# Kernel optimization log

Hardware: AMD Instinct MI355X
Metric: run time of the kernel (lower is better)

## Reference

```python
import jax, jax.numpy as jnp
import numpy as np
import math

NV, NC, NE = 25000, 12500, 250000
DV_LP = DC_LP = 16
D_IN = 128   # in_var_dim = in_con_dim = in_edge_dim
D_OUT = 128  # out_var_dim = out_con_dim = out_edge_dim
E_WO = 5
EDGE_IN = D_IN + 3 + E_WO       # 136 = num_edge_lp_f_with_ss(8) + in_edge_dim(128)
VAR_COMB = DV_LP + D_IN          # 144
CON_COMB = DC_LP + D_IN          # 144

def _lin(key, din, dout, bias=True):
    k1, k2 = jax.random.split(key)
    W = jax.random.normal(k1, (din, dout), jnp.float32) * 0.05
    if bias:
        return W, jax.random.normal(k2, (dout,), jnp.float32) * 0.05
    return W, None

def setup_inputs():
    key = jax.random.key(0)
    ks = iter(jax.random.split(key, 64))
    d = {}
    d["var_learned_f"] = jax.random.normal(next(ks), (NV, D_IN), jnp.float32)
    d["var_lp_f"] = jax.random.normal(next(ks), (NV, DV_LP), jnp.float32)
    d["con_learned_f"] = jax.random.normal(next(ks), (NC, D_IN), jnp.float32)
    d["con_lp_f"] = jax.random.normal(next(ks), (NC, DC_LP), jnp.float32)
    d["edge_learned_f"] = jax.random.normal(next(ks), (NE, D_IN), jnp.float32)
    d["lo_costs"] = jax.random.normal(next(ks), (NE,), jnp.float32)
    d["hi_costs"] = jax.random.normal(next(ks), (NE,), jnp.float32)
    d["def_mm"] = jax.random.normal(next(ks), (NE,), jnp.float32)
    d["edge_lp_f_wo_ss"] = jax.random.normal(next(ks), (NE, E_WO), jnp.float32)
    # con_updater TransformerConv: src=var_comb(144), dst=con_comb(144), edge(136) -> 128
    d["cu_Wq"], d["cu_bq"] = _lin(next(ks), CON_COMB, D_OUT)
    d["cu_Wk"], d["cu_bk"] = _lin(next(ks), VAR_COMB, D_OUT)
    d["cu_Wv"], d["cu_bv"] = _lin(next(ks), VAR_COMB, D_OUT)
    d["cu_We"], _ = _lin(next(ks), EDGE_IN, D_OUT, bias=False)
    d["cu_Ws"], d["cu_bs"] = _lin(next(ks), CON_COMB, D_OUT)
    # var_updater TransformerConv: src=new con_comb(144), dst=var_comb(144)
    d["vu_Wq"], d["vu_bq"] = _lin(next(ks), VAR_COMB, D_OUT)
    d["vu_Wk"], d["vu_bk"] = _lin(next(ks), CON_COMB, D_OUT)
    d["vu_Wv"], d["vu_bv"] = _lin(next(ks), CON_COMB, D_OUT)
    d["vu_We"], _ = _lin(next(ks), EDGE_IN, D_OUT, bias=False)
    d["vu_Ws"], d["vu_bs"] = _lin(next(ks), VAR_COMB, D_OUT)
    # EdgeUpdater MLPs (hidden = out_edge_dim = 128, num_hidden_layers_edge = 0)
    d["eu_vW1"], d["eu_vb1"] = _lin(next(ks), VAR_COMB, D_OUT)
    d["eu_vW2"], d["eu_vb2"] = _lin(next(ks), D_OUT, D_OUT)
    d["eu_cW1"], d["eu_cb1"] = _lin(next(ks), CON_COMB, D_OUT)
    d["eu_cW2"], d["eu_cb2"] = _lin(next(ks), D_OUT, D_OUT)
    d["eu_eW1"], d["eu_eb1"] = _lin(next(ks), EDGE_IN + 2 * D_OUT, D_OUT)
    d["eu_eW2"], d["eu_eb2"] = _lin(next(ks), D_OUT, D_OUT)
    d["edge_index_var"] = jax.random.randint(next(ks), (NE,), 0, NV)
    d["edge_index_con"] = jax.random.randint(next(ks), (NE,), 0, NC)
    return d

def transformer_conv(x_src, x_dst, src_idx, dst_idx, e,
                     Wq, bq, Wk, bk, Wv, bv, We, Ws, bs, n_dst):
    # PyG TransformerConv, heads=1, edge_dim, aggr='mean', root_weight=True
    C = Wq.shape[1]
    q = x_dst @ Wq + bq                      # [N_dst, C]
    k = x_src @ Wk + bk                      # [N_src, C]
    v = x_src @ Wv + bv
    ee = e @ We                              # [E, C] (lin_edge, no bias)
    kj = k[src_idx] + ee
    alpha = jnp.sum(q[dst_idx] * kj, axis=-1) * (1.0 / math.sqrt(C))  # [E]
    # segment softmax over destination nodes
    amax = jax.ops.segment_max(alpha, dst_idx, num_segments=n_dst)
    ex = jnp.exp(alpha - amax[dst_idx])
    denom = jax.ops.segment_sum(ex, dst_idx, num_segments=n_dst)
    a = ex / denom[dst_idx]
    msg = (v[src_idx] + ee) * a[:, None]
    agg = jax.ops.segment_sum(msg, dst_idx, num_segments=n_dst)
    cnt = jax.ops.segment_sum(jnp.ones_like(alpha), dst_idx, num_segments=n_dst)
    out = agg / jnp.maximum(cnt, 1.0)[:, None]   # aggr='mean'
    return out + x_dst @ Ws + bs                 # skip connection (lin_skip)

def _forward(var_learned_f, var_lp_f, con_learned_f, con_lp_f, edge_learned_f,
             lo_costs, hi_costs, def_mm, edge_lp_f_wo_ss,
             cu_Wq, cu_bq, cu_Wk, cu_bk, cu_Wv, cu_bv, cu_We, cu_Ws, cu_bs,
             vu_Wq, vu_bq, vu_Wk, vu_bk, vu_Wv, vu_bv, vu_We, vu_Ws, vu_bs,
             eu_vW1, eu_vb1, eu_vW2, eu_vb2, eu_cW1, eu_cb1, eu_cW2, eu_cb2,
             eu_eW1, eu_eb1, eu_eW2, eu_eb2,
             edge_index_var, edge_index_con):
    relu = jax.nn.relu
    var_comb = jnp.concatenate([var_learned_f, var_lp_f], axis=1)     # [NV,144]
    con_comb = jnp.concatenate([con_learned_f, con_lp_f], axis=1)     # [NC,144]
    edge_comb = jnp.concatenate([edge_learned_f, lo_costs[:, None], hi_costs[:, None],
                                 def_mm[:, None], edge_lp_f_wo_ss], axis=1)  # [NE,136]
    # con update: messages from vars (edge_index[0]) to cons (edge_index[1])
    con_new = relu(transformer_conv(var_comb, con_comb, edge_index_var, edge_index_con,
                                    edge_comb, cu_Wq, cu_bq, cu_Wk, cu_bk, cu_Wv, cu_bv,
                                    cu_We, cu_Ws, cu_bs, NC))
    con_comb = jnp.concatenate([con_new, con_lp_f], axis=1)
    # var update: flow target_to_source -> messages from cons (edge_index[1]) to vars (edge_index[0])
    var_new = relu(transformer_conv(con_comb, var_comb, edge_index_con, edge_index_var,
                                    edge_comb, vu_Wq, vu_bq, vu_Wk, vu_bk, vu_Wv, vu_bv,
                                    vu_We, vu_Ws, vu_bs, NV))
    var_comb = jnp.concatenate([var_new, var_lp_f], axis=1)
    # edge update: compress nodes, gather to edges, concat, MLP
    vc = relu(relu(var_comb @ eu_vW1 + eu_vb1) @ eu_vW2 + eu_vb2)     # [NV,128]
    cc = relu(relu(con_comb @ eu_cW1 + eu_cb1) @ eu_cW2 + eu_cb2)     # [NC,128]
    h = jnp.concatenate([edge_comb, vc[edge_index_var], cc[edge_index_con]], axis=1)  # [NE,392]
    edge_new = relu(relu(h @ eu_eW1 + eu_eb1) @ eu_eW2 + eu_eb2)
    return var_new, con_new, edge_new

def reference(var_learned_f, var_lp_f, con_learned_f, con_lp_f, edge_learned_f,
              lo_costs, hi_costs, def_mm, edge_lp_f_wo_ss,
              cu_Wq, cu_bq, cu_Wk, cu_bk, cu_Wv, cu_bv, cu_We, cu_Ws, cu_bs,
              vu_Wq, vu_bq, vu_Wk, vu_bk, vu_Wv, vu_bv, vu_We, vu_Ws, vu_bs,
              eu_vW1, eu_vb1, eu_vW2, eu_vb2, eu_cW1, eu_cb1, eu_cW2, eu_cb2,
              eu_eW1, eu_eb1, eu_eW2, eu_eb2,
              edge_index_var, edge_index_con):
    return _forward(var_learned_f, var_lp_f, con_learned_f, con_lp_f, edge_learned_f,
                    lo_costs, hi_costs, def_mm, edge_lp_f_wo_ss,
                    cu_Wq, cu_bq, cu_Wk, cu_bk, cu_Wv, cu_bv, cu_We, cu_Ws, cu_bs,
                    vu_Wq, vu_bq, vu_Wk, vu_bk, vu_Wv, vu_bv, vu_We, vu_Ws, vu_bs,
                    eu_vW1, eu_vb1, eu_vW2, eu_vb2, eu_cW1, eu_cb1, eu_cW2, eu_cb2,
                    eu_eW1, eu_eb1, eu_eW2, eu_eb2,
                    edge_index_var, edge_index_con)
```

## Files before the change

### kernel.cpp

```cpp
#include <hip/hip_runtime.h>
#include <math.h>

#define NVV 25000
#define NCC 12500
#define NEE 250000
#define KP 160

typedef short bf16x8 __attribute__((ext_vector_type(8)));
typedef float f32x4 __attribute__((ext_vector_type(4)));

__device__ __forceinline__ unsigned short f2bf(float f) {
  unsigned u = __float_as_uint(f);
  u += 0x7fffu + ((u >> 16) & 1u);
  return (unsigned short)(u >> 16);
}
__device__ __forceinline__ float bf2f(unsigned short u) {
  return __uint_as_float((unsigned)u << 16);
}
__device__ __forceinline__ void gll16(const unsigned short* g, unsigned short* l) {
  __builtin_amdgcn_global_load_lds(
      (const __attribute__((address_space(1))) unsigned int*)(const void*)g,
      (__attribute__((address_space(3))) unsigned int*)(void*)l, 16, 0, 0);
}

__device__ __forceinline__ void stage_rows64(const unsigned short* __restrict__ X,
                                             unsigned short* As, int row0, int N,
                                             int wave, int lane) {
  #pragma unroll
  for (int j = 0; j < 5; ++j) {
    int inst = wave * 5 + j;
    int L = inst * 1024 + lane * 16;
    int kk = L >> 12;
    int r = (L >> 6) & 63;
    int ks = (L & 63) >> 1;
    int grow = row0 + r; if (grow >= N) grow = N - 1;
    gll16(X + (size_t)grow * KP + kk * 32 + ks, As + inst * 512);
  }
}

template <int MI, int NI>
__device__ __forceinline__ void zero_acc(f32x4 (&acc)[MI][NI]) {
  #pragma unroll
  for (int mi = 0; mi < MI; ++mi)
    #pragma unroll
    for (int ni = 0; ni < NI; ++ni) {
      acc[mi][ni][0] = 0.f; acc[mi][ni][1] = 0.f;
      acc[mi][ni][2] = 0.f; acc[mi][ni][3] = 0.f;
    }
}

template <int MI, int NI>
__device__ __forceinline__ void chunk_mfma_g(const unsigned short* As,
                                             const unsigned short* __restrict__ WT,
                                             f32x4 (&acc)[MI][NI], int kk,
                                             int wm, int wn, int fr, int fq) {
  bf16x8 av[MI], bv[NI];
  #pragma unroll
  for (int mi = 0; mi < MI; ++mi)
    av[mi] = *(const bf16x8*)&As[kk * 2048 + (wm + mi * 16 + fr) * 32 + fq * 8];
  #pragma unroll
  for (int ni = 0; ni < NI; ++ni)
    bv[ni] = *(const bf16x8*)&WT[(size_t)(wn + ni * 16 + fr) * KP + kk * 32 + fq * 8];
  #pragma unroll
  for (int mi = 0; mi < MI; ++mi)
    #pragma unroll
    for (int ni = 0; ni < NI; ++ni)
      acc[mi][ni] = __builtin_amdgcn_mfma_f32_16x16x32_bf16(av[mi], bv[ni],
                                                            acc[mi][ni], 0, 0, 0);
}

struct GJob {
  const unsigned short* X; const unsigned short* WT;
  const float* bias; const float* addf;
  float* outf; unsigned short* outb;
  int outb_stride, pad_flag, N, relu_flag;
  int ntf;
};
struct GBatch { GJob j[4]; int start[4]; int njobs; };

__global__ __launch_bounds__(256, 4) void gemm_batch(GBatch B) {
  int job = 0;
  #pragma unroll
  for (int t = 1; t < 4; ++t)
    if (t < B.njobs && (int)blockIdx.x >= B.start[t]) job = t;
  GJob g = B.j[job];
  __shared__ unsigned short As[5 * 64 * 32];
  const int tid = threadIdx.x;
  const int lane = tid & 63, wave = tid >> 6;
  const int row0 = (blockIdx.x - B.start[job]) * 64;
  const int wm = (wave & 1) * 32, wn = (wave >> 1) * 64;
  const int fr = lane & 15, fq = lane >> 4;

  stage_rows64(g.X, As, row0, g.N, wave, lane);
  f32x4 acc[2][4];
  zero_acc<2, 4>(acc);
  __syncthreads();
  #pragma unroll
  for (int kk = 0; kk < 5; ++kk) chunk_mfma_g<2, 4>(As, g.WT, acc, kk, wm, wn, fr, fq);

  #pragma unroll
  for (int mi = 0; mi < 2; ++mi) {
    #pragma unroll
    for (int ni = 0; ni < 4; ++ni) {
      int gcol = wn + ni * 16 + fr;
      float bvv = g.bias ? g.bias[gcol] : 0.0f;
      #pragma unroll
      for (int r = 0; r < 4; ++r) {
        int grow = row0 + wm + mi * 16 + fq * 4 + r;
        if (grow < g.N) {
          float o = acc[mi][ni][r] + bvv;
          if (g.addf) o += g.addf[(size_t)grow * 128 + gcol];
          if (g.relu_flag) o = fmaxf(o, 0.f);
          if (g.outf) {
            if (g.ntf) __builtin_nontemporal_store(o, &g.outf[(size_t)grow * 128 + gcol]);
            else       g.outf[(size_t)grow * 128 + gcol] = o;
          }
          if (g.outb) g.outb[(size_t)grow * g.outb_stride + gcol] = f2bf(o);
        }
      }
    }
    if (g.outb && g.pad_flag && wn == 0) {
      #pragma unroll
      for (int r = 0; r < 4; ++r) {
        int grow = row0 + wm + mi * 16 + fq * 4 + r;
        if (grow < g.N)
          for (int pc = 128 + fr; pc < g.outb_stride; pc += 16)
            g.outb[(size_t)grow * g.outb_stride + pc] = 0;
      }
    }
  }
}

struct QTJob {
  const unsigned short* X; const unsigned short* Wq; const float* bq;
  const unsigned short* Wt; float* qf; unsigned short* tb; int N;
};
struct QTBatch { QTJob j[2]; int start; };

__global__ __launch_bounds__(256, 4) void gemm_qt(QTBatch B) {
  int job = ((int)blockIdx.x >= B.start) ? 1 : 0;
  QTJob g = B.j[job];
  __shared__ unsigned short As[5 * 64 * 32];
  const int tid = threadIdx.x;
  const int lane = tid & 63, wave = tid >> 6;
  const int row0 = (blockIdx.x - (job ? B.start : 0)) * 64;
  const int wm = (wave & 1) * 32;
  const int fr = lane & 15, fq = lane >> 4;

  stage_rows64(g.X, As, row0, g.N, wave, lane);
  {
    const int wn = (wave >> 1) * 64;
    f32x4 acc[2][4];
    zero_acc<2, 4>(acc);
    __syncthreads();
    #pragma unroll
    for (int kk = 0; kk < 5; ++kk) chunk_mfma_g<2, 4>(As, g.Wq, acc, kk, wm, wn, fr, fq);
    __syncthreads();
    #pragma unroll
    for (int mi = 0; mi < 2; ++mi)
      #pragma unroll
      for (int ni = 0; ni < 4; ++ni) {
        int col = wn + ni * 16 + fr;
        float bvv = g.bq[col];
        #pragma unroll
        for (int r = 0; r < 4; ++r) {
          int row = wm + mi * 16 + fq * 4 + r;
          int grow = row0 + row;
          float o = acc[mi][ni][r] + bvv;
          if (grow < g.N) g.qf[(size_t)grow * 128 + col] = o;
          As[(col >> 5) * 2048 + row * 32 + (col & 31)] = f2bf(o);
        }
      }
  }
  __syncthreads();
  {
    const int wn = (wave >> 1) * 80;
    f32x4 acc[2][5];
    zero_acc<2, 5>(acc);
    #pragma unroll
    for (int kk = 0; kk < 4; ++kk) chunk_mfma_g<2, 5>(As, g.Wt, acc, kk, wm, wn, fr, fq);
    #pragma unroll
    for (int mi = 0; mi < 2; ++mi)
      #pragma unroll
      for (int ni = 0; ni < 5; ++ni) {
        int gcol = wn + ni * 16 + fr;
        #pragma unroll
        for (int r = 0; r < 4; ++r) {
          int grow = row0 + wm + mi * 16 + fq * 4 + r;
          if (grow < g.N) g.tb[(size_t)grow * KP + gcol] = f2bf(acc[mi][ni][r]);
        }
      }
  }
}

__global__ __launch_bounds__(256, 4) void gemm_chain(
    const unsigned short* __restrict__ X,
    const unsigned short* __restrict__ W1, const float* __restrict__ b1,
    const unsigned short* __restrict__ W2, const float* __restrict__ b2,
    const unsigned short* __restrict__ W3,
    unsigned short* __restrict__ outw, int N) {
  __shared__ unsigned short As[5 * 64 * 32];
  const int tid = threadIdx.x;
  const int lane = tid & 63, wave = tid >> 6;
  const int row0 = blockIdx.x * 64;
  const int wm = (wave & 1) * 32, wn = (wave >> 1) * 64;
  const int fr = lane & 15, fq = lane >> 4;

  stage_rows64(X, As, row0, N, wave, lane);
  f32x4 acc[2][4];
  zero_acc<2, 4>(acc);
  __syncthreads();
  #pragma unroll
  for (int kk = 0; kk < 5; ++kk) chunk_mfma_g<2, 4>(As, W1, acc, kk, wm, wn, fr, fq);

  __syncthreads();
  #pragma unroll
  for (int mi = 0; mi < 2; ++mi)
    #pragma unroll
    for (int ni = 0; ni < 4; ++ni) {
      int col = wn + ni * 16 + fr;
      float bvv = b1[col];
      #pragma unroll
      for (int r = 0; r < 4; ++r) {
        int row = wm + mi * 16 + fq * 4 + r;
        float o = fmaxf(acc[mi][ni][r] + bvv, 0.f);
        As[(col >> 5) * 2048 + row * 32 + (col & 31)] = f2bf(o);
      }
    }
  zero_acc<2, 4>(acc);
  __syncthreads();

  #pragma unroll
  for (int kk = 0; kk < 4; ++kk) chunk_mfma_g<2, 4>(As, W2, acc, kk, wm, wn, fr, fq);

  __syncthreads();
  #pragma unroll
  for (int mi = 0; mi < 2; ++mi)
    #pragma unroll
    for (int ni = 0; ni < 4; ++ni) {
      int col = wn + ni * 16 + fr;
      float bvv = b2[col];
      #pragma unroll
      for (int r = 0; r < 4; ++r) {
        int row = wm + mi * 16 + fq * 4 + r;
        float o = fmaxf(acc[mi][ni][r] + bvv, 0.f);
        As[(col >> 5) * 2048 + row * 32 + (col & 31)] = f2bf(o);
      }
    }
  zero_acc<2, 4>(acc);
  __syncthreads();
  #pragma unroll
  for (int kk = 0; kk < 4; ++kk) chunk_mfma_g<2, 4>(As, W3, acc, kk, wm, wn, fr, fq);
  #pragma unroll
  for (int mi = 0; mi < 2; ++mi)
    #pragma unroll
    for (int ni = 0; ni < 4; ++ni) {
      int gcol = wn + ni * 16 + fr;
      #pragma unroll
      for (int r = 0; r < 4; ++r) {
        int grow = row0 + wm + mi * 16 + fq * 4 + r;
        if (grow < N) outw[(size_t)grow * 128 + gcol] = f2bf(acc[mi][ni][r]);
      }
    }
}

__device__ __forceinline__ void edge_epi(unsigned short* L, const f32x4 (&acc)[2][4],
    int rbase, int N, const float* __restrict__ b1,
    const unsigned short* __restrict__ gA, const unsigned short* __restrict__ gB,
    const int* __restrict__ giA, const int* __restrict__ giB,
    int wm, int wn, int fr, int fq) {
  #pragma unroll
  for (int mi = 0; mi < 2; ++mi)
    #pragma unroll
    for (int ni = 0; ni < 4; ++ni) {
      int col = wn + ni * 16 + fr;
      float bvv = b1[col];
      #pragma unroll
      for (int r = 0; r < 4; ++r) {
        int row = wm + mi * 16 + fq * 4 + r;
        int grow = rbase + row;
        int gi = (grow < N) ? grow : (N - 1);
        float o = acc[mi][ni][r] + bvv
                + bf2f(gA[(size_t)giA[gi] * 128 + col])
                + bf2f(gB[(size_t)giB[gi] * 128 + col]);
        o = fmaxf(o, 0.f);
        L[(col >> 5) * 2048 + row * 32 + (col & 31)] = f2bf(o);
      }
    }
}
__device__ __forceinline__ void edge_store(const f32x4 (&acc)[2][4], int rbase, int N,
    const float* __restrict__ b2, float* __restrict__ outf,
    int wm, int wn, int fr, int fq) {
  #pragma unroll
  for (int mi = 0; mi < 2; ++mi)
    #pragma unroll
    for (int ni = 0; ni < 4; ++ni) {
      int gcol = wn + ni * 16 + fr;
      float bvv = b2[gcol];
      #pragma unroll
      for (int r = 0; r < 4; ++r) {
        int grow = rbase + wm + mi * 16 + fq * 4 + r;
        if (grow < N) {
          float o = fmaxf(acc[mi][ni][r] + bvv, 0.f);
          __builtin_nontemporal_store(o, &outf[(size_t)grow * 128 + gcol]);
        }
      }
    }
}

__global__ __launch_bounds__(256, 4) void gemm_edge2(
    const unsigned short* __restrict__ X,
    const unsigned short* __restrict__ W1, const float* __restrict__ b1,
    const unsigned short* __restrict__ gA, const unsigned short* __restrict__ gB,
    const int* __restrict__ giA, const int* __restrict__ giB,
    const unsigned short* __restrict__ W2, const float* __restrict__ b2,
    float* __restrict__ outf, int N) {
  __shared__ unsigned short As[5 * 64 * 32];
  __shared__ unsigned short Bs[5 * 64 * 32];
  const int tid = threadIdx.x;
  const int lane = tid & 63, wave = tid >> 6;
  const int row0 = blockIdx.x * 128;
  const int wm = (wave & 1) * 32, wn = (wave >> 1) * 64;
  const int fr = lane & 15, fq = lane >> 4;

  stage_rows64(X, As, row0, N, wave, lane);
  f32x4 acc[2][4];
  zero_acc<2, 4>(acc);
  __syncthreads();
  stage_rows64(X, Bs, row0 + 64, N, wave, lane);

  #pragma unroll
  for (int kk = 0; kk < 5; ++kk) chunk_mfma_g<2, 4>(As, W1, acc, kk, wm, wn, fr, fq);
  __syncthreads();
  edge_epi(As, acc, row0, N, b1, gA, gB, giA, giB, wm, wn, fr, fq);
  zero_acc<2, 4>(acc);
  __syncthreads();
  #pragma unroll
  for (int kk = 0; kk < 4; ++kk) chunk_mfma_g<2, 4>(As, W2, acc, kk, wm, wn, fr, fq);
  edge_store(acc, row0, N, b2, outf, wm, wn, fr, fq);

  zero_acc<2, 4>(acc);
  #pragma unroll
  for (int kk = 0; kk < 5; ++kk) chunk_mfma_g<2, 4>(Bs, W1, acc, kk, wm, wn, fr, fq);
  __syncthreads();
  edge_epi(Bs, acc, row0 + 64, N, b1, gA, gB, giA, giB, wm, wn, fr, fq);
  zero_acc<2, 4>(acc);
  __syncthreads();
  #pragma unroll
  for (int kk = 0; kk < 4; ++kk) chunk_mfma_g<2, 4>(Bs, W2, acc, kk, wm, wn, fr, fq);
  edge_store(acc, row0 + 64, N, b2, outf, wm, wn, fr, fq);
}

__global__ void build_node_bf(const float* __restrict__ learned, const float* __restrict__ lp,
                              unsigned short* __restrict__ out, int N) {
  int idx = blockIdx.x * blockDim.x + threadIdx.x;
  if (idx >= N * 40) return;
  int row = idx / 40, c4 = idx - row * 40;
  int c = c4 * 4;
  ushort4 o;
  if (c4 < 32) {
    const float* p = learned + (size_t)row * 128 + c;
    o.x = f2bf(p[0]); o.y = f2bf(p[1]); o.z = f2bf(p[2]); o.w = f2bf(p[3]);
  } else if (c4 < 36) {
    const float* p = lp + (size_t)row * 16 + (c - 128);
    o.x = f2bf(p[0]); o.y = f2bf(p[1]); o.z = f2bf(p[2]); o.w = f2bf(p[3]);
  } else { o.x = o.y = o.z = o.w = 0; }
  *(ushort4*)&out[(size_t)row * KP + c] = o;
}

__global__ void build_edge_bf(const float* __restrict__ el, const float* __restrict__ lo,
                              const float* __restrict__ hi, const float* __restrict__ dm,
                              const float* __restrict__ wo, unsigned short* __restrict__ out) {
  int idx = blockIdx.x * blockDim.x + threadIdx.x;
  if (idx >= NEE * 40) return;
  int row = idx / 40, c4 = idx - row * 40;
  int c = c4 * 4;
  ushort4 o;
  if (c4 < 32) {
    const float* p = el + (size_t)row * 128 + c;
    o.x = f2bf(p[0]); o.y = f2bf(p[1]); o.z = f2bf(p[2]); o.w = f2bf(p[3]);
  } else if (c4 == 32) {
    o.x = f2bf(lo[row]); o.y = f2bf(hi[row]); o.z = f2bf(dm[row]);
    o.w = f2bf(wo[(size_t)row * 5 + 0]);
  } else if (c4 == 33) {
    const float* p = wo + (size_t)row * 5;
    o.x = f2bf(p[1]); o.y = f2bf(p[2]); o.z = f2bf(p[3]); o.w = f2bf(p[4]);
  } else { o.x = o.y = o.z = o.w = 0; }
  *(ushort4*)&out[(size_t)row * KP + c] = o;
}

struct WJobs {
  const float* W[20];
  unsigned short* O[20];
  int K[20];
  int TR[20];
};
__global__ void convert_weights(WJobs j) {
  int b = blockIdx.x;
  int job = b / 100;
  int i = (b - job * 100) * 256 + threadIdx.x;
  int col = i / KP;
  int k = i - col * KP;
  float v = 0.f;
  if (j.TR[job]) { if (col < 128 && k < j.K[job]) v = j.W[job][(size_t)k * 128 + col]; }
  else           { if (col < 136 && k < j.K[job]) v = j.W[job][(size_t)col * 128 + k]; }
  j.O[job][(size_t)col * KP + k] = f2bf(v);
}

__global__ void zero2(int* __restrict__ a, int na, int* __restrict__ b, int nb) {
  int i = blockIdx.x * blockDim.x + threadIdx.x;
  if (i < na) a[i] = 0;
  if (i < nb) b[i] = 0;
}
__global__ void hist2(const int* __restrict__ dc, int* __restrict__ cc,
                      const int* __restrict__ dv, int* __restrict__ cv, int nE) {
  int e = blockIdx.x * blockDim.x + threadIdx.x;
  if (e >= nE) return;
  atomicAdd(&cc[dc[e]], 1);
  atomicAdd(&cv[dv[e]], 1);
}
__global__ void csr_scan(const int* __restrict__ counts, int* __restrict__ offsets,
                         int* __restrict__ cursor, int n) {
  __shared__ int part[256];
  int tid = threadIdx.x;
  int chunk = (n + 255) / 256;
  int lo = tid * chunk, hi = min(n, lo + chunk);
  int s = 0;
  for (int i = lo; i < hi; ++i) s += counts[i];
  part[tid] = s;
  __syncthreads();
  if (tid == 0) {
    int run = 0;
    for (int i = 0; i < 256; ++i) { int t = part[i]; part[i] = run; run += t; }
    offsets[n] = run;
  }
  __syncthreads();
  int base = part[tid];
  for (int i = lo; i < hi; ++i) { offsets[i] = base; cursor[i] = base; base += counts[i]; }
}
__global__ void csr_scatter(const int* __restrict__ dst, const int* __restrict__ src,
                            int* __restrict__ cursor, int2* __restrict__ ces, int nE) {
  int e = blockIdx.x * blockDim.x + threadIdx.x;
  if (e >= nE) return;
  int pos = atomicAdd(&cursor[dst[e]], 1);
  ces[pos] = make_int2(e, src[e]);
}

struct AttSt { float m, l, ax, ay, axe, aye, axe2, aye2; };
__device__ __forceinline__ void att_upd(AttSt& s, float alpha, unsigned vu,
                                        float e0, float e1, float e2, float e3) {
  float mn = fmaxf(s.m, alpha);
  float scale = __expf(s.m - mn);
  float w = __expf(alpha - mn);
  s.ax = s.ax * scale + __uint_as_float(vu << 16) * w;
  s.ay = s.ay * scale + __uint_as_float(vu & 0xffff0000u) * w;
  s.axe = s.axe * scale + e0 * w;   s.aye = s.aye * scale + e1 * w;
  s.axe2 = s.axe2 * scale + e2 * w; s.aye2 = s.aye2 * scale + e3 * w;
  s.l = s.l * scale + w; s.m = mn;
}

__global__ void fused_attn(
    const float* __restrict__ qbuf, const unsigned short* __restrict__ kbuf,
    const unsigned short* __restrict__ vbuf, const unsigned short* __restrict__ tbuf,
    const unsigned short* __restrict__ ecomb,
    const int* __restrict__ offsets, const int2* __restrict__ ces,
    float* __restrict__ accVS, unsigned short* __restrict__ accE, int Nd) {
  int d = blockIdx.x * 4 + (threadIdx.x >> 6);
  if (d >= Nd) return;
  int lane = threadIdx.x & 63;
  int c = lane * 2;
  bool tl = (lane < 16);
  int c2 = 128 + c;
  float2 qv = *(const float2*)&qbuf[(size_t)d * 128 + c];
  unsigned tu = *(const unsigned*)&tbuf[(size_t)d * KP + c];
  float tx = __uint_as_float(tu << 16);
  float ty = __uint_as_float(tu & 0xffff0000u);
  float tx2 = 0.f, ty2 = 0.f;
  if (tl) {
    unsigned tu2 = *(const unsigned*)&tbuf[(size_t)d * KP + c2];
    tx2 = __uint_as_float(tu2 << 16);
    ty2 = __uint_as_float(tu2 & 0xffff0000u);
  }
  int beg = offsets[d], end = offsets[d + 1];
  AttSt st{-INFINITY, 0.f, 0.f, 0.f, 0.f, 0.f, 0.f, 0.f};
  const float SC = 0.08838834764831845f;
  int i = beg;
  for (; i + 3 < end; i += 4) {
    int2 pr[4];
    pr[0] = ces[i]; pr[1] = ces[i + 1]; pr[2] = ces[i + 2]; pr[3] = ces[i + 3];
    unsigned eu[4], ku[4], vu[4];
    float e0[4], e1[4], e2[4], e3[4], p[4];
    #pragma unroll
    for (int u = 0; u < 4; ++u) {
      eu[u] = *(const unsigned*)&ecomb[(size_t)pr[u].x * KP + c];
      ku[u] = *(const unsigned*)&kbuf[(size_t)pr[u].y * 128 + c];
      vu[u] = *(const unsigned*)&vbuf[(size_t)pr[u].y * 128 + c];
    }
    #pragma unroll
    for (int u = 0; u < 4; ++u) {
      e0[u] = __uint_as_float(eu[u] << 16);
      e1[u] = __uint_as_float(eu[u] & 0xffff0000u);
      e2[u] = 0.f; e3[u] = 0.f;
    }
    if (tl) {
      #pragma unroll
      for (int u = 0; u < 4; ++u) {
        unsigned x = *(const unsigned*)&ecomb[(size_t)pr[u].x * KP + c2];
        e2[u] = __uint_as_float(x << 16);
        e3[u] = __uint_as_float(x & 0xffff0000u);
      }
    }
    #pragma unroll
    for (int u = 0; u < 4; ++u)
      p[u] = qv.x * __uint_as_float(ku[u] << 16) + qv.y * __uint_as_float(ku[u] & 0xffff0000u)
           + tx * e0[u] + ty * e1[u] + tx2 * e2[u] + ty2 * e3[u];
    #pragma unroll
    for (int off = 1; off < 64; off <<= 1) {
      p[0] += __shfl_xor(p[0], off, 64);
      p[1] += __shfl_xor(p[1], off, 64);
      p[2] += __shfl_xor(p[2], off, 64);
      p[3] += __shfl_xor(p[3], off, 64);
    }
    #pragma unroll
    for (int u = 0; u < 4; ++u)
      att_upd(st, p[u] * SC, vu[u], e0[u], e1[u], e2[u], e3[u]);
  }
  for (; i < end; ++i) {
    int2 pr = ces[i];
    unsigned eu = *(const unsigned*)&ecomb[(size_t)pr.x * KP + c];
    float e0 = __uint_as_float(eu << 16);
    float e1 = __uint_as_float(eu & 0xffff0000u);
    float e2 = 0.f, e3 = 0.f;
    if (tl) {
      unsigned x = *(const unsigned*)&ecomb[(size_t)pr.x * KP + c2];
      e2 = __uint_as_float(x << 16);
      e3 = __uint_as_float(x & 0xffff0000u);
    }
    unsigned ku = *(const unsigned*)&kbuf[(size_t)pr.y * 128 + c];
    unsigned vu = *(const unsigned*)&vbuf[(size_t)pr.y * 128 + c];
    float p = qv.x * __uint_as_float(ku << 16) + qv.y * __uint_as_float(ku & 0xffff0000u)
            + tx * e0 + ty * e1 + tx2 * e2 + ty2 * e3;
    #pragma unroll
    for (int off = 1; off < 64; off <<= 1) p += __shfl_xor(p, off, 64);
    att_upd(st, p * SC, vu, e0, e1, e2, e3);
  }
  int deg = end - beg;
  float inv = (deg > 0) ? 1.0f / (st.l * (float)deg) : 0.0f;
  float2 sk = *(const float2*)&accVS[(size_t)d * 128 + c];
  *(float2*)&accVS[(size_t)d * 128 + c] =
      make_float2(st.ax * inv + sk.x, st.ay * inv + sk.y);
  ushort2 oe; oe.x = f2bf(st.axe * inv); oe.y = f2bf(st.aye * inv);
  *(ushort2*)&accE[(size_t)d * KP + c] = oe;
  if (tl) {
    ushort2 oe2; oe2.x = f2bf(st.axe2 * inv); oe2.y = f2bf(st.aye2 * inv);
    *(ushort2*)&accE[(size_t)d * KP + c2] = oe2;
  }
}

extern "C" void kernel_launch(void* const* d_in, const int* in_sizes, int n_in,
                              void* d_out, int out_size, void* d_ws, size_t ws_size,
                              hipStream_t stream) {
  const float* var_learned = (const float*)d_in[0];
  const float* var_lp      = (const float*)d_in[1];
  const float* con_learned = (const float*)d_in[2];
  const float* con_lp      = (const float*)d_in[3];
  const float* edge_learned= (const float*)d_in[4];
  const float* lo          = (const float*)d_in[5];
  const float* hi          = (const float*)d_in[6];
  const float* dm          = (const float*)d_in[7];
  const float* wo          = (const float*)d_in[8];
  const float* cu_Wq = (const float*)d_in[9],  *cu_bq = (const float*)d_in[10];
  const float* cu_Wk = (const float*)d_in[11], *cu_bk = (const float*)d_in[12];
  const float* cu_Wv = (const float*)d_in[13], *cu_bv = (const float*)d_in[14];
  const float* cu_We = (const float*)d_in[15];
  const float* cu_Ws = (const float*)d_in[16], *cu_bs = (const float*)d_in[17];
  const float* vu_Wq = (const float*)d_in[18], *vu_bq = (const float*)d_in[19];
  const float* vu_Wk = (const float*)d_in[20], *vu_bk = (const float*)d_in[21];
  const float* vu_Wv = (const float*)d_in[22], *vu_bv = (const float*)d_in[23];
  const float* vu_We = (const float*)d_in[24];
  const float* vu_Ws = (const float*)d_in[25], *vu_bs = (const float*)d_in[26];
  const float* eu_vW1 = (const float*)d_in[27], *eu_vb1 = (const float*)d_in[28];
  const float* eu_vW2 = (const float*)d_in[29], *eu_vb2 = (const float*)d_in[30];
  const float* eu_cW1 = (const float*)d_in[31], *eu_cb1 = (const float*)d_in[32];
  const float* eu_cW2 = (const float*)d_in[33], *eu_cb2 = (const float*)d_in[34];
  const float* eu_eW1 = (const float*)d_in[35], *eu_eb1 = (const float*)d_in[36];
  const float* eu_eW2 = (const float*)d_in[37], *eu_eb2 = (const float*)d_in[38];
  const int* eiv = (const int*)d_in[39];
  const int* eic = (const int*)d_in[40];

  float* out_var  = (float*)d_out;
  float* out_con  = out_var + (size_t)NVV * 128;
  float* out_edge = out_con + (size_t)NCC * 128;

  char* w = (char*)d_ws;
  auto alloc = [&](size_t bytes) { char* p = w; w += (bytes + 255) & ~(size_t)255; return p; };
  unsigned short* edge_comb_bf = (unsigned short*)alloc((size_t)NEE * KP * 2);
  unsigned short* var_comb_bf = (unsigned short*)alloc((size_t)NVV * KP * 2);
  unsigned short* con_comb_bf = (unsigned short*)alloc((size_t)NCC * KP * 2);
  unsigned short* t_bfA   = (unsigned short*)alloc((size_t)NCC * KP * 2);
  unsigned short* t_bfB   = (unsigned short*)alloc((size_t)NVV * KP * 2);
  unsigned short* accE_bf = (unsigned short*)alloc((size_t)NVV * KP * 2);
  unsigned short* kv_bf   = (unsigned short*)alloc((size_t)NVV * 128 * 2);
  unsigned short* vv_bf   = (unsigned short*)alloc((size_t)NVV * 128 * 2);
  unsigned short* vc_bf   = (unsigned short*)alloc((size_t)NVV * 128 * 2);
  unsigned short* cc_bf   = (unsigned short*)alloc((size_t)NCC * 128 * 2);
  float* bufV1 = (float*)alloc((size_t)NVV * 128 * 4);
  float* bufV2 = (float*)alloc((size_t)NVV * 128 * 4);
  float* bufC1 = (float*)alloc((size_t)NCC * 128 * 4);
  float* bufC2 = (float*)alloc((size_t)NCC * 128 * 4);
  unsigned short* WTbase = (unsigned short*)alloc((size_t)20 * 160 * KP * 2);
  int* countsC = (int*)alloc((size_t)NCC * 4);
  int* countsV = (int*)alloc((size_t)NVV * 4);
  int* offC = (int*)alloc((size_t)(NCC + 1) * 4);
  int* curC = (int*)alloc((size_t)NCC * 4);
  int* offV = (int*)alloc((size_t)(NVV + 1) * 4);
  int* curV = (int*)alloc((size_t)NVV * 4);
  int2* cesA = (int2*)alloc((size_t)NEE * 8);
  int2* cesB = (int2*)alloc((size_t)NEE * 8);
  (void)ws_size; (void)in_sizes; (void)n_in; (void)out_size;

  unsigned short* WT[20];
  for (int i = 0; i < 20; ++i) WT[i] = WTbase + (size_t)i * 160 * KP;
  WJobs jobs;
  const float* Wsrc[20] = {cu_Wq, cu_Wk, cu_Wv, cu_We, cu_Ws,
                           vu_Wq, vu_Wk, vu_Wv, vu_We, vu_Ws,
                           eu_vW1, eu_vW2, eu_cW1, eu_cW2,
                           eu_eW1, eu_eW1 + 136 * 128, eu_eW1 + 264 * 128, eu_eW2,
                           cu_We, vu_We};
  const int Ksrc[20] = {144, 144, 144, 136, 144, 144, 144, 144, 136, 144,
                        144, 128, 144, 128, 136, 128, 128, 128, 128, 128};
  const int Tsrc[20] = {1,1,1,1,1, 1,1,1,1,1, 1,1,1,1, 1,1,1,1, 0,0};
  for (int i = 0; i < 20; ++i) {
    jobs.W[i] = Wsrc[i]; jobs.O[i] = WT[i]; jobs.K[i] = Ksrc[i]; jobs.TR[i] = Tsrc[i];
  }

  const int T = 256;
  const int NBC = (NCC + 63) / 64;
  const int NBV = (NVV + 63) / 64;
  const int NBE2 = (NEE + 127) / 128;

  build_node_bf<<<(NVV * 40 + T - 1) / T, T, 0, stream>>>(var_learned, var_lp, var_comb_bf, NVV);
  build_node_bf<<<(NCC * 40 + T - 1) / T, T, 0, stream>>>(con_learned, con_lp, con_comb_bf, NCC);
  build_edge_bf<<<(NEE * 40 + T - 1) / T, T, 0, stream>>>(edge_learned, lo, hi, dm, wo, edge_comb_bf);
  convert_weights<<<20 * 100, T, 0, stream>>>(jobs);

  zero2<<<(NVV + T - 1) / T, T, 0, stream>>>(countsC, NCC, countsV, NVV);
  hist2<<<(NEE + T - 1) / T, T, 0, stream>>>(eic, countsC, eiv, countsV, NEE);
  csr_scan<<<1, 256, 0, stream>>>(countsC, offC, curC, NCC);
  csr_scan<<<1, 256, 0, stream>>>(countsV, offV, curV, NVV);
  csr_scatter<<<(NEE + T - 1) / T, T, 0, stream>>>(eic, eiv, curC, cesA, NEE);
  csr_scatter<<<(NEE + T - 1) / T, T, 0, stream>>>(eiv, eic, curV, cesB, NEE);

  {
    QTBatch b{};
    b.j[0] = {con_comb_bf, WT[0], cu_bq, WT[18], bufC1, t_bfA, NCC};
    b.j[1] = {var_comb_bf, WT[5], vu_bq, WT[19], bufV1, t_bfB, NVV};
    b.start = NBC;
    gemm_qt<<<NBC + NBV, 256, 0, stream>>>(b);
  }

  {
    GBatch b{};
    b.j[0] = {con_comb_bf, WT[4], cu_bs, nullptr, bufC2, nullptr, 0, 0, NCC, 0, 0};
    b.j[1] = {var_comb_bf, WT[1], cu_bk, nullptr, nullptr, kv_bf, 128, 0, NVV, 0, 0};
    b.j[2] = {var_comb_bf, WT[2], cu_bv, nullptr, nullptr, vv_bf, 128, 0, NVV, 0, 0};
    b.start[0] = 0; b.start[1] = NBC; b.start[2] = NBC + NBV;
    b.njobs = 3;
    gemm_batch<<<NBC + 2 * NBV, 256, 0, stream>>>(b);
  }
  fused_attn<<<(NCC + 3) / 4, 256, 0, stream>>>(bufC1, kv_bf, vv_bf, t_bfA, edge_comb_bf,
                                                offC, cesA, bufC2, accE_bf, NCC);
  {
    GBatch b{};
    b.j[0] = {accE_bf, WT[3], nullptr, bufC2, out_con, con_comb_bf, KP, 0, NCC, 1, 1};
    b.start[0] = 0; b.njobs = 1;
    gemm_batch<<<NBC, 256, 0, stream>>>(b);
  }

  {
    GBatch b{};
    b.j[0] = {var_comb_bf, WT[9], vu_bs, nullptr, bufV2, nullptr, 0, 0, NVV, 0, 0};
    b.j[1] = {con_comb_bf, WT[6], vu_bk, nullptr, nullptr, kv_bf, 128, 0, NCC, 0, 0};
    b.j[2] = {con_comb_bf, WT[7], vu_bv, nullptr, nullptr, vv_bf, 128, 0, NCC, 0, 0};
    b.start[0] = 0; b.start[1] = NBV; b.start[2] = NBV + NBC;
    b.njobs = 3;
    gemm_batch<<<NBV + 2 * NBC, 256, 0, stream>>>(b);
  }
  fused_attn<<<(NVV + 3) / 4, 256, 0, stream>>>(bufV1, kv_bf, vv_bf, t_bfB, edge_comb_bf,
                                                offV, cesB, bufV2, accE_bf, NVV);
  {
    GBatch b{};
    b.j[0] = {accE_bf, WT[8], nullptr, bufV2, out_var, var_comb_bf, KP, 0, NVV, 1, 1};
    b.start[0] = 0; b.njobs = 1;
    gemm_batch<<<NBV, 256, 0, stream>>>(b);
  }

  gemm_chain<<<NBV, 256, 0, stream>>>(
      var_comb_bf, WT[10], eu_vb1, WT[11], eu_vb2, WT[15], vc_bf, NVV);
  gemm_chain<<<NBC, 256, 0, stream>>>(
      con_comb_bf, WT[12], eu_cb1, WT[13], eu_cb2, WT[16], cc_bf, NCC);
  gemm_edge2<<<NBE2, 256, 0, stream>>>(
      edge_comb_bf, WT[14], eu_eb1, vc_bf, cc_bf, eiv, eic,
      WT[17], eu_eb2, out_edge, NEE);
}
```

Baseline: 775.3 us.

## Fuse node output projection with K/V and edge-MLP chain into one kernel

Replaces the separate output-projection GEMM, the following K/V GEMMs and the per-node edge-MLP chain with a single node_update kernel. It keeps the freshly computed node features (with the lp columns) in LDS and runs the K/V and MLP GEMMs from there. Hoists all input-independent projections (Q/T, skip, first K/V) into one six-job launch, and folds bias and gather terms into the accumulator initialisation. This removes several launches and the global round trip of the combined node features, at the cost of a longer serial kernel per block with more syncs.

```diff
diff --git a/kernel.cpp b/kernel.cpp
--- a/kernel.cpp
+++ b/kernel.cpp
@@ -69,136 +69,112 @@
                                                             acc[mi][ni], 0, 0, 0);
 }
 
-struct GJob {
-  const unsigned short* X; const unsigned short* WT;
-  const float* bias; const float* addf;
-  float* outf; unsigned short* outb;
-  int outb_stride, pad_flag, N, relu_flag;
-  int ntf;
+__device__ __forceinline__ void init_bias(f32x4 (&acc)[2][4], const float* __restrict__ b,
+                                          int wn, int fr) {
+  #pragma unroll
+  for (int ni = 0; ni < 4; ++ni) {
+    float bvv = b[wn + ni * 16 + fr];
+    #pragma unroll
+    for (int mi = 0; mi < 2; ++mi) {
+      acc[mi][ni][0] = bvv; acc[mi][ni][1] = bvv;
+      acc[mi][ni][2] = bvv; acc[mi][ni][3] = bvv;
+    }
+  }
+}
+
+struct MJob {
+  const unsigned short* X; const unsigned short* W1; const float* b1;
+  const unsigned short* Wt;
+  float* outf; unsigned short* outb; unsigned short* tb;
+  int N;
 };
-struct GBatch { GJob j[4]; int start[4]; int njobs; };
-
-__global__ __launch_bounds__(256, 4) void gemm_batch(GBatch B) {
+struct MBatch { MJob j[6]; int start[6]; int njobs; };
+
+__global__ __launch_bounds__(256, 4) void gemm_multi(MBatch B) {
   int job = 0;
   #pragma unroll
-  for (int t = 1; t < 4; ++t)
+  for (int t = 1; t < 6; ++t)
     if (t < B.njobs && (int)blockIdx.x >= B.start[t]) job = t;
-  GJob g = B.j[job];
+  MJob g = B.j[job];
   __shared__ unsigned short As[5 * 64 * 32];
   const int tid = threadIdx.x;
   const int lane = tid & 63, wave = tid >> 6;
   const int row0 = (blockIdx.x - B.start[job]) * 64;
-  const int wm = (wave & 1) * 32, wn = (wave >> 1) * 64;
-  const int fr = lane & 15, fq = lane >> 4;
-
-  stage_rows64(g.X, As, row0, g.N, wave, lane);
-  f32x4 acc[2][4];
-  zero_acc<2, 4>(acc);
-  __syncthreads();
-  #pragma unroll
-  for (int kk = 0; kk < 5; ++kk) chunk_mfma_g<2, 4>(As, g.WT, acc, kk, wm, wn, fr, fq);
-
-  #pragma unroll
-  for (int mi = 0; mi < 2; ++mi) {
-    #pragma unroll
-    for (int ni = 0; ni < 4; ++ni) {
-      int gcol = wn + ni * 16 + fr;
-      float bvv = g.bias ? g.bias[gcol] : 0.0f;
-      #pragma unroll
-      for (int r = 0; r < 4; ++r) {
-        int grow = row0 + wm + mi * 16 + fq * 4 + r;
-        if (grow < g.N) {
-          float o = acc[mi][ni][r] + bvv;
-          if (g.addf) o += g.addf[(size_t)grow * 128 + gcol];
-          if (g.relu_flag) o = fmaxf(o, 0.f);
-          if (g.outf) {
-            if (g.ntf) __builtin_nontemporal_store(o, &g.outf[(size_t)grow * 128 + gcol]);
-            else       g.outf[(size_t)grow * 128 + gcol] = o;
-          }
-          if (g.outb) g.outb[(size_t)grow * g.outb_stride + gcol] = f2bf(o);
-        }
-      }
-    }
-    if (g.outb && g.pad_flag && wn == 0) {
-      #pragma unroll
-      for (int r = 0; r < 4; ++r) {
-        int grow = row0 + wm + mi * 16 + fq * 4 + r;
-        if (grow < g.N)
-          for (int pc = 128 + fr; pc < g.outb_stride; pc += 16)
-            g.outb[(size_t)grow * g.outb_stride + pc] = 0;
-      }
-    }
-  }
-}
-
-struct QTJob {
-  const unsigned short* X; const unsigned short* Wq; const float* bq;
-  const unsigned short* Wt; float* qf; unsigned short* tb; int N;
-};
-struct QTBatch { QTJob j[2]; int start; };
-
-__global__ __launch_bounds__(256, 4) void gemm_qt(QTBatch B) {
-  int job = ((int)blockIdx.x >= B.start) ? 1 : 0;
-  QTJob g = B.j[job];
-  __shared__ unsigned short As[5 * 64 * 32];
-  const int tid = threadIdx.x;
-  const int lane = tid & 63, wave = tid >> 6;
-  const int row0 = (blockIdx.x - (job ? B.start : 0)) * 64;
   const int wm = (wave & 1) * 32;
   const int fr = lane & 15, fq = lane >> 4;
 
   stage_rows64(g.X, As, row0, g.N, wave, lane);
-  {
-    const int wn = (wave >> 1) * 64;
-    f32x4 acc[2][4];
-    zero_acc<2, 4>(acc);
-    __syncthreads();
-    #pragma unroll
-    for (int kk = 0; kk < 5; ++kk) chunk_mfma_g<2, 4>(As, g.Wq, acc, kk, wm, wn, fr, fq);
+  const int wn = (wave >> 1) * 64;
+  f32x4 acc[2][4];
+  init_bias(acc, g.b1, wn, fr);
+  __syncthreads();
+  #pragma unroll
+  for (int kk = 0; kk < 5; ++kk) chunk_mfma_g<2, 4>(As, g.W1, acc, kk, wm, wn, fr, fq);
+
+  if (!g.Wt) {
+    #pragma unroll
+    for (int mi = 0; mi < 2; ++mi)
+      #pragma unroll
+      for (int ni = 0; ni < 4; ++ni) {
+        int gcol = wn + ni * 16 + fr;
+        #pragma unroll
+        for (int r = 0; r < 4; ++r) {
+          int grow = row0 + wm + mi * 16 + fq * 4 + r;
+          if (grow < g.N) {
+            float o = acc[mi][ni][r];
+            if (g.outf) g.outf[(size_t)grow * 128 + gcol] = o;
+            if (g.outb) g.outb[(size_t)grow * 128 + gcol] = f2bf(o);
+          }
+        }
+      }
+  } else {
     __syncthreads();
     #pragma unroll
     for (int mi = 0; mi < 2; ++mi)
       #pragma unroll
       for (int ni = 0; ni < 4; ++ni) {
         int col = wn + ni * 16 + fr;
-        float bvv = g.bq[col];
         #pragma unroll
         for (int r = 0; r < 4; ++r) {
           int row = wm + mi * 16 + fq * 4 + r;
           int grow = row0 + row;
-          float o = acc[mi][ni][r] + bvv;
-          if (grow < g.N) g.qf[(size_t)grow * 128 + col] = o;
+          float o = acc[mi][ni][r];
+          if (grow < g.N) g.outf[(size_t)grow * 128 + col] = o;
           As[(col >> 5) * 2048 + row * 32 + (col & 31)] = f2bf(o);
         }
       }
-  }
-  __syncthreads();
-  {
-    const int wn = (wave >> 1) * 80;
-    f32x4 acc[2][5];
-    zero_acc<2, 5>(acc);
-    #pragma unroll
-    for (int kk = 0; kk < 4; ++kk) chunk_mfma_g<2, 5>(As, g.Wt, acc, kk, wm, wn, fr, fq);
+    __syncthreads();
+    const int wn5 = (wave >> 1) * 80;
+    f32x4 acc2[2][5];
+    zero_acc<2, 5>(acc2);
+    #pragma unroll
+    for (int kk = 0; kk < 4; ++kk) chunk_mfma_g<2, 5>(As, g.Wt, acc2, kk, wm, wn5, fr, fq);
     #pragma unroll
     for (int mi = 0; mi < 2; ++mi)
       #pragma unroll
       for (int ni = 0; ni < 5; ++ni) {
-        int gcol = wn + ni * 16 + fr;
+        int gcol = wn5 + ni * 16 + fr;
         #pragma unroll
         for (int r = 0; r < 4; ++r) {
           int grow = row0 + wm + mi * 16 + fq * 4 + r;
-          if (grow < g.N) g.tb[(size_t)grow * KP + gcol] = f2bf(acc[mi][ni][r]);
+          if (grow < g.N) g.tb[(size_t)grow * KP + gcol] = f2bf(acc2[mi][ni][r]);
         }
       }
   }
 }
 
-__global__ __launch_bounds__(256, 4) void gemm_chain(
-    const unsigned short* __restrict__ X,
-    const unsigned short* __restrict__ W1, const float* __restrict__ b1,
-    const unsigned short* __restrict__ W2, const float* __restrict__ b2,
-    const unsigned short* __restrict__ W3,
-    unsigned short* __restrict__ outw, int N) {
+__global__ __launch_bounds__(256, 4) void node_update(
+    const unsigned short* __restrict__ accE, const float* __restrict__ accVS,
+    const float* __restrict__ lp,
+    const unsigned short* __restrict__ We, float* __restrict__ outF,
+    const unsigned short* __restrict__ Wk, const float* __restrict__ bk,
+    unsigned short* __restrict__ kout,
+    const unsigned short* __restrict__ Wv, const float* __restrict__ bv,
+    unsigned short* __restrict__ vout,
+    const unsigned short* __restrict__ C1, const float* __restrict__ c1b,
+    const unsigned short* __restrict__ C2, const float* __restrict__ c2b,
+    const unsigned short* __restrict__ C3, unsigned short* __restrict__ cout,
+    int N) {
   __shared__ unsigned short As[5 * 64 * 32];
   const int tid = threadIdx.x;
   const int lane = tid & 63, wave = tid >> 6;
@@ -206,14 +182,136 @@
   const int wm = (wave & 1) * 32, wn = (wave >> 1) * 64;
   const int fr = lane & 15, fq = lane >> 4;
 
-  stage_rows64(X, As, row0, N, wave, lane);
+  int lrow = row0 + (tid >> 2); if (lrow >= N) lrow = N - 1;
+  float4 lpv = *(const float4*)&lp[(size_t)lrow * 16 + (tid & 3) * 4];
+
+  stage_rows64(accE, As, row0, N, wave, lane);
+
   f32x4 acc[2][4];
+  #pragma unroll
+  for (int mi = 0; mi < 2; ++mi)
+    #pragma unroll
+    for (int ni = 0; ni < 4; ++ni) {
+      int col = wn + ni * 16 + fr;
+      #pragma unroll
+      for (int r = 0; r < 4; ++r) {
+        int grow = row0 + wm + mi * 16 + fq * 4 + r;
+        int gi = (grow < N) ? grow : (N - 1);
+        acc[mi][ni][r] = accVS[(size_t)gi * 128 + col];
+      }
+    }
+  __syncthreads();
+  #pragma unroll
+  for (int kk = 0; kk < 5; ++kk) chunk_mfma_g<2, 4>(As, We, acc, kk, wm, wn, fr, fq);
+  __syncthreads();
+
+  #pragma unroll
+  for (int mi = 0; mi < 2; ++mi)
+    #pragma unroll
+    for (int ni = 0; ni < 4; ++ni) {
+      int col = wn + ni * 16 + fr;
+      #pragma unroll
+      for (int r = 0; r < 4; ++r) {
+        int row = wm + mi * 16 + fq * 4 + r;
+        int grow = row0 + row;
+        float o = fmaxf(acc[mi][ni][r], 0.f);
+        if (grow < N) __builtin_nontemporal_store(o, &outF[(size_t)grow * 128 + col]);
+        As[(col >> 5) * 2048 + row * 32 + (col & 31)] = f2bf(o);
+      }
+    }
+  {
+    int r = tid >> 2, cb = (tid & 3) * 4;
+    unsigned short* p = &As[4 * 2048 + r * 32 + cb];
+    p[0] = f2bf(lpv.x); p[1] = f2bf(lpv.y); p[2] = f2bf(lpv.z); p[3] = f2bf(lpv.w);
+  }
+  __syncthreads();
+
+  if (Wk) {
+    init_bias(acc, bk, wn, fr);
+    #pragma unroll
+    for (int kk = 0; kk < 5; ++kk) chunk_mfma_g<2, 4>(As, Wk, acc, kk, wm, wn, fr, fq);
+    #pragma unroll
+    for (int mi = 0; mi < 2; ++mi)
+      #pragma unroll
+      for (int ni = 0; ni < 4; ++ni) {
+        int gcol = wn + ni * 16 + fr;
+        #pragma unroll
+        for (int r = 0; r < 4; ++r) {
+          int grow = row0 + wm + mi * 16 + fq * 4 + r;
+          if (grow < N) kout[(size_t)grow * 128 + gcol] = f2bf(acc[mi][ni][r]);
+        }
+      }
+    init_bias(acc, bv, wn, fr);
+    #pragma unroll
+    for (int kk = 0; kk < 5; ++kk) chunk_mfma_g<2, 4>(As, Wv, acc, kk, wm, wn, fr, fq);
+    #pragma unroll
+    for (int mi = 0; mi < 2; ++mi)
+      #pragma unroll
+      for (int ni = 0; ni < 4; ++ni) {
+        int gcol = wn + ni * 16 + fr;
+        #pragma unroll
+        for (int r = 0; r < 4; ++r) {
+          int grow = row0 + wm + mi * 16 + fq * 4 + r;
+          if (grow < N) vout[(size_t)grow * 128 + gcol] = f2bf(acc[mi][ni][r]);
+        }
+      }
+  }
+
+  init_bias(acc, c1b, wn, fr);
+  #pragma unroll
+  for (int kk = 0; kk < 5; ++kk) chunk_mfma_g<2, 4>(As, C1, acc, kk, wm, wn, fr, fq);
+  __syncthreads();
+  #pragma unroll
+  for (int mi = 0; mi < 2; ++mi)
+    #pragma unroll
+    for (int ni = 0; ni < 4; ++ni) {
+      int col = wn + ni * 16 + fr;
+      #pragma unroll
+      for (int r = 0; r < 4; ++r) {
+        int row = wm + mi * 16 + fq * 4 + r;
+        float o = fmaxf(acc[mi][ni][r], 0.f);
+        As[(col >> 5) * 2048 + row * 32 + (col & 31)] = f2bf(o);
+      }
+    }
+  __syncthreads();
+  init_bias(acc, c2b, wn, fr);
+  #pragma unroll
+  for (int kk = 0; kk < 4; ++kk) chunk_mfma_g<2, 4>(As, C2, acc, kk, wm, wn, fr, fq);
+  __syncthreads();
+  #pragma unroll
+  for (int mi = 0; mi < 2; ++mi)
+    #pragma unroll
+    for (int ni = 0; ni < 4; ++ni) {
+      int col = wn + ni * 16 + fr;
+      #pragma unroll
+      for (int r = 0; r < 4; ++r) {
+        int row = wm + mi * 16 + fq * 4 + r;
+        float o = fmaxf(acc[mi][ni][r], 0.f);
+        As[(col >> 5) * 2048 + row * 32 + (col & 31)] = f2bf(o);
+      }
+    }
+  __syncthreads();
   zero_acc<2, 4>(acc);
-  __syncthreads();
-  #pragma unroll
-  for (int kk = 0; kk < 5; ++kk) chunk_mfma_g<2, 4>(As, W1, acc, kk, wm, wn, fr, fq);
-
-  __syncthreads();
+  #pragma unroll
+  for (int kk = 0; kk < 4; ++kk) chunk_mfma_g<2, 4>(As, C3, acc, kk, wm, wn, fr, fq);
+  #pragma unroll
+  for (int mi = 0; mi < 2; ++mi)
+    #pragma unroll
+    for (int ni = 0; ni < 4; ++ni) {
+      int gcol = wn + ni * 16 + fr;
+      #pragma unroll
+      for (int r = 0; r < 4; ++r) {
+        int grow = row0 + wm + mi * 16 + fq * 4 + r;
+        if (grow < N) cout[(size_t)grow * 128 + gcol] = f2bf(acc[mi][ni][r]);
+      }
+    }
+}
+
+__device__ __forceinline__ void init_gather(f32x4 (&acc)[2][4], int rbase, int N,
+    const float* __restrict__ b1,
+    const unsigned short* __restrict__ gA, const unsigned short* __restrict__ gB,
+    const int* __restrict__ giA, const int* __restrict__ giB,
+    int wm, int wn, int fr, int fq) {
   #pragma unroll
   for (int mi = 0; mi < 2; ++mi)
     #pragma unroll
@@ -222,68 +320,24 @@
       float bvv = b1[col];
       #pragma unroll
       for (int r = 0; r < 4; ++r) {
-        int row = wm + mi * 16 + fq * 4 + r;
-        float o = fmaxf(acc[mi][ni][r] + bvv, 0.f);
-        As[(col >> 5) * 2048 + row * 32 + (col & 31)] = f2bf(o);
-      }
-    }
-  zero_acc<2, 4>(acc);
-  __syncthreads();
-
-  #pragma unroll
-  for (int kk = 0; kk < 4; ++kk) chunk_mfma_g<2, 4>(As, W2, acc, kk, wm, wn, fr, fq);
-
-  __syncthreads();
+        int grow = rbase + wm + mi * 16 + fq * 4 + r;
+        int gi = (grow < N) ? grow : (N - 1);
+        acc[mi][ni][r] = bvv + bf2f(gA[(size_t)giA[gi] * 128 + col])
+                             + bf2f(gB[(size_t)giB[gi] * 128 + col]);
+      }
+    }
+}
+__device__ __forceinline__ void epi_relu_lds(unsigned short* L, const f32x4 (&acc)[2][4],
+    int wm, int wn, int fr, int fq) {
   #pragma unroll
   for (int mi = 0; mi < 2; ++mi)
     #pragma unroll
     for (int ni = 0; ni < 4; ++ni) {
       int col = wn + ni * 16 + fr;
-      float bvv = b2[col];
       #pragma unroll
       for (int r = 0; r < 4; ++r) {
         int row = wm + mi * 16 + fq * 4 + r;
-        float o = fmaxf(acc[mi][ni][r] + bvv, 0.f);
-        As[(col >> 5) * 2048 + row * 32 + (col & 31)] = f2bf(o);
-      }
-    }
-  zero_acc<2, 4>(acc);
-  __syncthreads();
-  #pragma unroll
-  for (int kk = 0; kk < 4; ++kk) chunk_mfma_g<2, 4>(As, W3, acc, kk, wm, wn, fr, fq);
-  #pragma unroll
-  for (int mi = 0; mi < 2; ++mi)
-    #pragma unroll
-    for (int ni = 0; ni < 4; ++ni) {
-      int gcol = wn + ni * 16 + fr;
-      #pragma unroll
-      for (int r = 0; r < 4; ++r) {
-        int grow = row0 + wm + mi * 16 + fq * 4 + r;
-        if (grow < N) outw[(size_t)grow * 128 + gcol] = f2bf(acc[mi][ni][r]);
-      }
-    }
-}
-
-__device__ __forceinline__ void edge_epi(unsigned short* L, const f32x4 (&acc)[2][4],
-    int rbase, int N, const float* __restrict__ b1,
-    const unsigned short* __restrict__ gA, const unsigned short* __restrict__ gB,
-    const int* __restrict__ giA, const int* __restrict__ giB,
-    int wm, int wn, int fr, int fq) {
-  #pragma unroll
-  for (int mi = 0; mi < 2; ++mi)
-    #pragma unroll
-    for (int ni = 0; ni < 4; ++ni) {
-      int col = wn + ni * 16 + fr;
-      float bvv = b1[col];
-      #pragma unroll
-      for (int r = 0; r < 4; ++r) {
-        int row = wm + mi * 16 + fq * 4 + r;
-        int grow = rbase + row;
-        int gi = (grow < N) ? grow : (N - 1);
-        float o = acc[mi][ni][r] + bvv
-                + bf2f(gA[(size_t)giA[gi] * 128 + col])
-                + bf2f(gB[(size_t)giB[gi] * 128 + col]);
-        o = fmaxf(o, 0.f);
+        float o = fmaxf(acc[mi][ni][r], 0.f);
         L[(col >> 5) * 2048 + row * 32 + (col & 31)] = f2bf(o);
       }
     }
@@ -325,25 +379,25 @@
 
   stage_rows64(X, As, row0, N, wave, lane);
   f32x4 acc[2][4];
-  zero_acc<2, 4>(acc);
+  init_gather(acc, row0, N, b1, gA, gB, giA, giB, wm, wn, fr, fq);
   __syncthreads();
   stage_rows64(X, Bs, row0 + 64, N, wave, lane);
 
   #pragma unroll
   for (int kk = 0; kk < 5; ++kk) chunk_mfma_g<2, 4>(As, W1, acc, kk, wm, wn, fr, fq);
   __syncthreads();
-  edge_epi(As, acc, row0, N, b1, gA, gB, giA, giB, wm, wn, fr, fq);
+  epi_relu_lds(As, acc, wm, wn, fr, fq);
   zero_acc<2, 4>(acc);
   __syncthreads();
   #pragma unroll
   for (int kk = 0; kk < 4; ++kk) chunk_mfma_g<2, 4>(As, W2, acc, kk, wm, wn, fr, fq);
   edge_store(acc, row0, N, b2, outf, wm, wn, fr, fq);
 
-  zero_acc<2, 4>(acc);
+  init_gather(acc, row0 + 64, N, b1, gA, gB, giA, giB, wm, wn, fr, fq);
   #pragma unroll
   for (int kk = 0; kk < 5; ++kk) chunk_mfma_g<2, 4>(Bs, W1, acc, kk, wm, wn, fr, fq);
   __syncthreads();
-  edge_epi(Bs, acc, row0 + 64, N, b1, gA, gB, giA, giB, wm, wn, fr, fq);
+  epi_relu_lds(Bs, acc, wm, wn, fr, fq);
   zero_acc<2, 4>(acc);
   __syncthreads();
   #pragma unroll
@@ -652,53 +706,34 @@
   csr_scatter<<<(NEE + T - 1) / T, T, 0, stream>>>(eiv, eic, curV, cesB, NEE);
 
   {
-    QTBatch b{};
-    b.j[0] = {con_comb_bf, WT[0], cu_bq, WT[18], bufC1, t_bfA, NCC};
-    b.j[1] = {var_comb_bf, WT[5], vu_bq, WT[19], bufV1, t_bfB, NVV};
-    b.start = NBC;
-    gemm_qt<<<NBC + NBV, 256, 0, stream>>>(b);
-  }
-
-  {
-    GBatch b{};
-    b.j[0] = {con_comb_bf, WT[4], cu_bs, nullptr, bufC2, nullptr, 0, 0, NCC, 0, 0};
-    b.j[1] = {var_comb_bf, WT[1], cu_bk, nullptr, nullptr, kv_bf, 128, 0, NVV, 0, 0};
-    b.j[2] = {var_comb_bf, WT[2], cu_bv, nullptr, nullptr, vv_bf, 128, 0, NVV, 0, 0};
+    MBatch b{};
+    b.j[0] = {con_comb_bf, WT[0], cu_bq, WT[18], bufC1, nullptr, t_bfA, NCC};
+    b.j[1] = {var_comb_bf, WT[5], vu_bq, WT[19], bufV1, nullptr, t_bfB, NVV};
+    b.j[2] = {con_comb_bf, WT[4], cu_bs, nullptr, bufC2, nullptr, nullptr, NCC};
+    b.j[3] = {var_comb_bf, WT[9], vu_bs, nullptr, bufV2, nullptr, nullptr, NVV};
+    b.j[4] = {var_comb_bf, WT[1], cu_bk, nullptr, nullptr, kv_bf, nullptr, NVV};
+    b.j[5] = {var_comb_bf, WT[2], cu_bv, nullptr, nullptr, vv_bf, nullptr, NVV};
     b.start[0] = 0; b.start[1] = NBC; b.start[2] = NBC + NBV;
-    b.njobs = 3;
-    gemm_batch<<<NBC + 2 * NBV, 256, 0, stream>>>(b);
-  }
+    b.start[3] = 2 * NBC + NBV; b.start[4] = 2 * NBC + 2 * NBV;
+    b.start[5] = 2 * NBC + 3 * NBV;
+    b.njobs = 6;
+    gemm_multi<<<2 * NBC + 4 * NBV, 256, 0, stream>>>(b);
+  }
+
   fused_attn<<<(NCC + 3) / 4, 256, 0, stream>>>(bufC1, kv_bf, vv_bf, t_bfA, edge_comb_bf,
                                                 offC, cesA, bufC2, accE_bf, NCC);
-  {
-    GBatch b{};
-    b.j[0] = {accE_bf, WT[3], nullptr, bufC2, out_con, con_comb_bf, KP, 0, NCC, 1, 1};
-    b.start[0] = 0; b.njobs = 1;
-    gemm_batch<<<NBC, 256, 0, stream>>>(b);
-  }
-
-  {
-    GBatch b{};
-    b.j[0] = {var_comb_bf, WT[9], vu_bs, nullptr, bufV2, nullptr, 0, 0, NVV, 0, 0};
-    b.j[1] = {con_comb_bf, WT[6], vu_bk, nullptr, nullptr, kv_bf, 128, 0, NCC, 0, 0};
-    b.j[2] = {con_comb_bf, WT[7], vu_bv, nullptr, nullptr, vv_bf, 128, 0, NCC, 0, 0};
-    b.start[0] = 0; b.start[1] = NBV; b.start[2] = NBV + NBC;
-    b.njobs = 3;
-    gemm_batch<<<NBV + 2 * NBC, 256, 0, stream>>>(b);
-  }
+  node_update<<<NBC, 256, 0, stream>>>(
+      accE_bf, bufC2, con_lp, WT[3], out_con,
+      WT[6], vu_bk, kv_bf, WT[7], vu_bv, vv_bf,
+      WT[12], eu_cb1, WT[13], eu_cb2, WT[16], cc_bf, NCC);
+
   fused_attn<<<(NVV + 3) / 4, 256, 0, stream>>>(bufV1, kv_bf, vv_bf, t_bfB, edge_comb_bf,
                                                 offV, cesB, bufV2, accE_bf, NVV);
-  {
-    GBatch b{};
-    b.j[0] = {accE_bf, WT[8], nullptr, bufV2, out_var, var_comb_bf, KP, 0, NVV, 1, 1};
-    b.start[0] = 0; b.njobs = 1;
-    gemm_batch<<<NBV, 256, 0, stream>>>(b);
-  }
-
-  gemm_chain<<<NBV, 256, 0, stream>>>(
-      var_comb_bf, WT[10], eu_vb1, WT[11], eu_vb2, WT[15], vc_bf, NVV);
-  gemm_chain<<<NBC, 256, 0, stream>>>(
-      con_comb_bf, WT[12], eu_cb1, WT[13], eu_cb2, WT[16], cc_bf, NCC);
+  node_update<<<NBV, 256, 0, stream>>>(
+      accE_bf, bufV2, var_lp, WT[8], out_var,
+      nullptr, nullptr, nullptr, nullptr, nullptr, nullptr,
+      WT[10], eu_vb1, WT[11], eu_vb2, WT[15], vc_bf, NVV);
+
   gemm_edge2<<<NBE2, 256, 0, stream>>>(
       edge_comb_bf, WT[14], eu_eb1, vc_bf, cc_bf, eiv, eic,
       WT[17], eu_eb2, out_edge, NEE);
```

Measured after the change: 741.4 us. 4.4% less time.
